# Kernel tuning notes

Measured on AMD Instinct MI355X. Metric: run time of the kernel, lower is better.

The kernel has to match this reference:

```python
import jax, jax.numpy as jnp
import numpy as np

B, S, E = 8, 4096, 128
H, O = 64, 64  # attention_hidden_dim, out_dim


def setup_inputs() -> dict:
    key = jax.random.key(0)
    ks = jax.random.split(key, 4)
    x = jax.random.normal(ks[0], (B, S, E), dtype=jnp.float32)
    Wq = jax.random.normal(ks[1], (E, H), dtype=jnp.float32) * (1.0 / np.sqrt(E))
    Wk = jax.random.normal(ks[2], (E, H), dtype=jnp.float32) * (1.0 / np.sqrt(E))
    Wv = jax.random.normal(ks[3], (E, O), dtype=jnp.float32) * (1.0 / np.sqrt(E))
    bq = jnp.zeros((H,), dtype=jnp.float32)
    bk = jnp.zeros((H,), dtype=jnp.float32)
    bv = jnp.zeros((O,), dtype=jnp.float32)
    return {"x": x, "Wq": Wq, "bq": bq, "Wk": Wk, "bk": bk, "Wv": Wv, "bv": bv}


def reference(x, Wq, bq, Wk, bk, Wv, bv):
    # Batched version of the per-sample loop: q = x@Wq+bq, etc.
    q = jnp.einsum("bse,eh->bsh", x, Wq) + bq   # [B,S,H]
    k = jnp.einsum("bse,eh->bsh", x, Wk) + bk   # [B,S,H]
    v = jnp.einsum("bse,eo->bso", x, Wv) + bv   # [B,S,O]
    scores = jnp.einsum("bqh,bkh->bqk", q, k)   # QK^T per sample, [B,S,S]
    attn = jax.nn.softmax(scores, axis=-1)       # softmax over key dim
    out = jnp.einsum("bqk,bko->bqo", attn, v)   # [B,S,O]
    return out
```

## Files before the change

### kernel.cpp

```cpp
#include <hip/hip_runtime.h>
#include <math.h>

#define BB 8
#define SS 4096
#define EE 128
#define HH 64
#define NT 16
#define LOG2E 1.44269504088896f

typedef _Float16 f16;
typedef __attribute__((ext_vector_type(8))) _Float16 f16x8;
typedef __attribute__((ext_vector_type(4))) float f32x4;

__device__ __forceinline__ unsigned int pk2h(float a, float b) {
    return __builtin_bit_cast(unsigned int, __builtin_amdgcn_cvt_pkrtz(a, b));
}

__device__ __forceinline__ void tile_barrier() {
    asm volatile("s_waitcnt lgkmcnt(0)" ::: "memory");
    __builtin_amdgcn_s_barrier();
    __builtin_amdgcn_sched_barrier(0);
}

__global__ __launch_bounds__(256) void wtrans_kernel(
    const float* __restrict__ Wq, const float* __restrict__ Wk,
    const float* __restrict__ Wv, f16* __restrict__ Wt)
{
    const int idx = blockIdx.x * 256 + threadIdx.x;
    if (idx >= 192 * 128) return;
    const int col = idx >> 7, e = idx & 127;
    const float v = (col < 64)  ? Wq[e * 64 + col] * LOG2E
                  : (col < 128) ? Wk[e * 64 + (col - 64)]
                                : Wv[e * 64 + (col - 128)];
    Wt[col * 128 + e] = (f16)v;
}

__global__ __launch_bounds__(256) void qkv_kernel(
    const float* __restrict__ x, const f16* __restrict__ Wt,
    const float* __restrict__ bq, const float* __restrict__ bk,
    const float* __restrict__ bv,
    f16* __restrict__ Q, f16* __restrict__ K, f16* __restrict__ Vt)
{
    __shared__ __align__(16) short xs[64 * EE];
    const int tid = threadIdx.x;
    const long rowbase = (long)blockIdx.x * 64;

    {
        const float4* xg = (const float4*)(x + rowbase * EE);
#pragma unroll
        for (int j = 0; j < 8; ++j) {
            const int eidx = tid * 32 + j * 4;
            const float4 v = xg[eidx >> 2];
            unsigned long long pk =
                (unsigned long long)pk2h(v.x, v.y) |
                ((unsigned long long)pk2h(v.z, v.w) << 32);
            const int row = eidx >> 7;
            const int off = (row * 256 + (eidx & 127) * 2) ^ ((row & 7) << 4);
            *(unsigned long long*)((char*)xs + off) = pk;
        }
    }
    __syncthreads();

    const int lane = tid & 63;
    const int wid  = tid >> 6;
    const int ln15 = lane & 15;
    const int lg   = lane >> 4;

    f16x8 xa[4];
    {
        const int row = wid * 16 + ln15;
        const int swz = (row & 7) << 4;
#pragma unroll
        for (int s = 0; s < 4; ++s)
            xa[s] = *(const f16x8*)((const char*)xs + ((row * 256 + lg * 16 + s * 64) ^ swz));
    }

    f32x4 acc[12];
#pragma unroll
    for (int ct = 0; ct < 12; ++ct) acc[ct] = (f32x4){0.f, 0.f, 0.f, 0.f};

#pragma unroll
    for (int ct = 0; ct < 12; ++ct) {
        const f16* wtp = Wt + (ct * 16 + ln15) * 128 + lg * 8;
#pragma unroll
        for (int s = 0; s < 4; ++s) {
            const f16x8 wb = *(const f16x8*)(wtp + s * 32);
            acc[ct] = __builtin_amdgcn_mfma_f32_16x16x32_f16(xa[s], wb, acc[ct], 0, 0, 0);
        }
    }

    const long grow0 = rowbase + wid * 16 + 4 * lg;
#pragma unroll
    for (int ct = 0; ct < 4; ++ct) {
        const int col = ct * 16 + ln15;
        const float b = bq[col] * LOG2E;
#pragma unroll
        for (int r = 0; r < 4; ++r)
            Q[(grow0 + r) * HH + col] = (f16)(acc[ct][r] + b);
    }
#pragma unroll
    for (int ct = 4; ct < 8; ++ct) {
        const int col = (ct - 4) * 16 + ln15;
        const float b = bk[col];
#pragma unroll
        for (int r = 0; r < 4; ++r)
            K[(grow0 + r) * HH + col] = (f16)(acc[ct][r] + b);
    }
    {
        const long batch = rowbase >> 12;
        const long inrow = (rowbase & 4095) + wid * 16 + 4 * lg;
#pragma unroll
        for (int ct = 8; ct < 12; ++ct) {
            const int o = (ct - 8) * 16 + ln15;
            const float b = bv[o];
            unsigned long long pk =
                (unsigned long long)pk2h(acc[ct][0] + b, acc[ct][1] + b) |
                ((unsigned long long)pk2h(acc[ct][2] + b, acc[ct][3] + b) << 32);
            *(unsigned long long*)(Vt + ((long)batch * HH + o) * SS + inrow) = pk;
        }
    }
}

__global__ __launch_bounds__(256, 4) void flash_kernel(
    const f16* __restrict__ Q, const f16* __restrict__ K,
    const f16* __restrict__ Vt, f16* __restrict__ Onorm,
    float* __restrict__ lse)
{
    __shared__ __align__(16) short k_s[2][64 * HH];
    __shared__ __align__(16) short v_s[2][64 * HH];
    __shared__ __align__(16) short p_s[4 * 16 * HH];

    const int tid  = threadIdx.x;
    const int lane = tid & 63;
    const int wid  = tid >> 6;
    const int ln15 = lane & 15;
    const int lg   = lane >> 4;
    const int batch = blockIdx.x & 7;
    const int rest  = blockIdx.x >> 3;
    const int split = rest & 3;
    const int qtile = rest >> 2;
    const int k0base = split * (SS / 4);

    f16x8 qf[2];
    {
        const long qrow = (long)batch * SS + qtile * 64 + wid * 16 + ln15;
        const f16* qp = Q + qrow * HH + lg * 8;
        qf[0] = *(const f16x8*)(qp);
        qf[1] = *(const f16x8*)(qp + 32);
    }

    f32x4 oacc[4];
#pragma unroll
    for (int ot = 0; ot < 4; ++ot) oacc[ot] = (f32x4){0.f, 0.f, 0.f, 0.f};
    float m = -1e30f, l = 0.f;

    short* pw = p_s + wid * (16 * HH);
    const int swq = (ln15 & 7) << 4;

    const int row0 = tid >> 3;
    const int row1 = row0 + 32;
    const int cc0  = (tid & 7) * 16;
    const int dk0 = (row0 * 128 + cc0) ^ ((row0 & 7) << 4);
    const int dk1 = (row1 * 128 + cc0) ^ ((row1 & 7) << 4);

    const uint4* kb  = (const uint4*)(K + ((long)batch * SS + k0base) * HH);
    const f16* vbase = Vt + (long)batch * HH * SS + k0base + (tid & 7) * 8;

    uint4 kA0, kA1, vA0, vA1, kB0, kB1, vB0, vB1;

#define LOADT(t, k0r, k1r, v0r, v1r)                                   \
    do {                                                               \
        const uint4* kp = kb + (t) * 512 + tid;                        \
        k0r = kp[0];                                                   \
        k1r = kp[256];                                                 \
        const f16* vp = vbase + (t) * 64 + (long)row0 * SS;            \
        v0r = *(const uint4*)vp;                                       \
        v1r = *(const uint4*)(vp + 32 * SS);                           \
    } while (0)

#define WRITET(buf, k0r, k1r, v0r, v1r)                                \
    do {                                                               \
        *(uint4*)((char*)k_s[buf] + dk0) = k0r;                        \
        *(uint4*)((char*)k_s[buf] + dk1) = k1r;                        \
        *(uint4*)((char*)v_s[buf] + dk0) = v0r;                        \
        *(uint4*)((char*)v_s[buf] + dk1) = v1r;                        \
    } while (0)

    auto compute = [&](int cur) __attribute__((always_inline)) {
        const short* ks = k_s[cur];
        const short* vs = v_s[cur];

        f32x4 sacc[4];
        __builtin_amdgcn_s_setprio(1);
#pragma unroll
        for (int kt = 0; kt < 4; ++kt) {
            f32x4 a = (f32x4){0.f, 0.f, 0.f, 0.f};
            const int key = kt * 16 + ln15;
            const int rb = key * 128, swz = (key & 7) << 4;
            const f16x8 ka0 = *(const f16x8*)((const char*)ks + ((rb + lg * 16) ^ swz));
            const f16x8 ka1 = *(const f16x8*)((const char*)ks + ((rb + lg * 16 + 64) ^ swz));
            a = __builtin_amdgcn_mfma_f32_16x16x32_f16(ka0, qf[0], a, 0, 0, 0);
            a = __builtin_amdgcn_mfma_f32_16x16x32_f16(ka1, qf[1], a, 0, 0, 0);
            sacc[kt] = a;
        }
        __builtin_amdgcn_s_setprio(0);

        float t0 = fmaxf(fmaxf(sacc[0][0], sacc[0][1]), sacc[0][2]);
        float t1 = fmaxf(fmaxf(sacc[0][3], sacc[1][0]), sacc[1][1]);
        float t2 = fmaxf(fmaxf(sacc[1][2], sacc[1][3]), sacc[2][0]);
        float t3 = fmaxf(fmaxf(sacc[2][1], sacc[2][2]), sacc[2][3]);
        float t4 = fmaxf(fmaxf(sacc[3][0], sacc[3][1]), sacc[3][2]);
        float tm = fmaxf(fmaxf(fmaxf(t0, t1), t2), fmaxf(fmaxf(t3, t4), sacc[3][3]));
        tm = fmaxf(tm, __shfl_xor(tm, 16));
        tm = fmaxf(tm, __shfl_xor(tm, 32));
        if (!__all(tm <= m + 11.5f)) {
            const float mn = fmaxf(m, tm);
            const float alpha = __builtin_amdgcn_exp2f(m - mn);
            l *= alpha;
#pragma unroll
            for (int r = 0; r < 4; ++r) {
                const float ar = __shfl(alpha, lg * 4 + r);
                oacc[0][r] *= ar; oacc[1][r] *= ar;
                oacc[2][r] *= ar; oacc[3][r] *= ar;
            }
            m = mn;
        }

        float ps = 0.f;
#pragma unroll
        for (int kt = 0; kt < 4; ++kt)
#pragma unroll
            for (int r = 0; r < 4; ++r) {
                const float pv = __builtin_amdgcn_exp2f(sacc[kt][r] - m);
                sacc[kt][r] = pv;
                ps += pv;
            }
        ps += __shfl_xor(ps, 16);
        ps += __shfl_xor(ps, 32);
        l += ps;

#pragma unroll
        for (int kt = 0; kt < 4; ++kt) {
            uint2 pk;
            pk.x = pk2h(sacc[kt][0], sacc[kt][1]);
            pk.y = pk2h(sacc[kt][2], sacc[kt][3]);
            const int key = kt * 16 + lg * 4;
            *(uint2*)((char*)pw + ((ln15 * 128 + key * 2) ^ swq)) = pk;
        }

        __builtin_amdgcn_s_setprio(1);
#pragma unroll
        for (int s = 0; s < 2; ++s) {
            const f16x8 pa = *(const f16x8*)((const char*)pw + ((ln15 * 128 + lg * 16 + s * 64) ^ swq));
#pragma unroll
            for (int ot = 0; ot < 4; ++ot) {
                const int o = ot * 16 + ln15;
                const f16x8 vb = *(const f16x8*)((const char*)vs + ((o * 128 + lg * 16 + s * 64) ^ ((o & 7) << 4)));
                oacc[ot] = __builtin_amdgcn_mfma_f32_16x16x32_f16(pa, vb, oacc[ot], 0, 0, 0);
            }
        }
        __builtin_amdgcn_s_setprio(0);
    };

    LOADT(0, kA0, kA1, vA0, vA1);
    WRITET(0, kA0, kA1, vA0, vA1);
    LOADT(1, kA0, kA1, vA0, vA1);
    __syncthreads();

    for (int t = 0; t < NT; t += 2) {
        compute(0);
        if (t + 2 < NT) LOADT(t + 2, kB0, kB1, vB0, vB1);
        WRITET(1, kA0, kA1, vA0, vA1);
        tile_barrier();

        compute(1);
        if (t + 3 < NT) LOADT(t + 3, kA0, kA1, vA0, vA1);
        if (t + 2 < NT) WRITET(0, kB0, kB1, vB0, vB1);
        tile_barrier();
    }
#undef LOADT
#undef WRITET

    const float linv = 1.0f / l;
    const long ridx = (long)split * (BB * SS) + (long)batch * SS + qtile * 64 + wid * 16;
#pragma unroll
    for (int r = 0; r < 4; ++r) {
        const float ir = __shfl(linv, lg * 4 + r);
        f16* op = Onorm + (ridx + lg * 4 + r) * HH + ln15;
        op[0]  = (f16)(oacc[0][r] * ir);
        op[16] = (f16)(oacc[1][r] * ir);
        op[32] = (f16)(oacc[2][r] * ir);
        op[48] = (f16)(oacc[3][r] * ir);
    }
    if (lg == 0)
        lse[ridx + ln15] = m + __builtin_amdgcn_logf(l);
}

__global__ __launch_bounds__(256) void merge_kernel(
    const f16* __restrict__ Onorm, const float* __restrict__ lse,
    float* __restrict__ Out)
{
    const int gid = blockIdx.x * 256 + threadIdx.x;
    const long row = gid >> 3;
    const int c0 = (gid & 7) * 8;
    const long NR = (long)BB * SS;

    float ls[4];
#pragma unroll
    for (int i = 0; i < 4; ++i) ls[i] = lse[i * NR + row];
    const float M = fmaxf(fmaxf(ls[0], ls[1]), fmaxf(ls[2], ls[3]));
    float g[4], denom = 0.f;
#pragma unroll
    for (int i = 0; i < 4; ++i) { g[i] = __builtin_amdgcn_exp2f(ls[i] - M); denom += g[i]; }
    const float inv = 1.0f / denom;

    float acc[8];
#pragma unroll
    for (int j = 0; j < 8; ++j) acc[j] = 0.f;
#pragma unroll
    for (int i = 0; i < 4; ++i) {
        const f16x8 o = *(const f16x8*)(Onorm + (i * NR + row) * HH + c0);
#pragma unroll
        for (int j = 0; j < 8; ++j) acc[j] = fmaf(g[i], (float)o[j], acc[j]);
    }
    float4 r0, r1;
    r0.x = acc[0] * inv; r0.y = acc[1] * inv; r0.z = acc[2] * inv; r0.w = acc[3] * inv;
    r1.x = acc[4] * inv; r1.y = acc[5] * inv; r1.z = acc[6] * inv; r1.w = acc[7] * inv;
    float4* dst = (float4*)(Out + row * HH + c0);
    dst[0] = r0;
    dst[1] = r1;
}

extern "C" void kernel_launch(void* const* d_in, const int* in_sizes, int n_in,
                              void* d_out, int out_size, void* d_ws, size_t ws_size,
                              hipStream_t stream) {
    const float* x  = (const float*)d_in[0];
    const float* Wq = (const float*)d_in[1];
    const float* bq = (const float*)d_in[2];
    const float* Wk = (const float*)d_in[3];
    const float* bk = (const float*)d_in[4];
    const float* Wv = (const float*)d_in[5];
    const float* bv = (const float*)d_in[6];
    float* out = (float*)d_out;

    const size_t NTOK = (size_t)BB * SS;
    f16* Q  = (f16*)d_ws;
    f16* K  = Q + NTOK * HH;
    f16* Vt = K + NTOK * HH;
    f16* Wt = Vt + NTOK * HH;
    f16* Onorm = Wt + 192 * 128;
    float* lse = (float*)(Onorm + 4 * NTOK * HH);

    wtrans_kernel<<<96, 256, 0, stream>>>(Wq, Wk, Wv, Wt);
    qkv_kernel<<<BB * SS / 64, 256, 0, stream>>>(x, Wt, bq, bk, bv, Q, K, Vt);
    flash_kernel<<<BB * 4 * (SS / 64), 256, 0, stream>>>(Q, K, Vt, Onorm, lse);
    merge_kernel<<<BB * SS * 8 / 256, 256, 0, stream>>>(Onorm, lse, out);
}
```

Baseline: 89.11 us.

## Stream K/V tiles directly into LDS with async global_load_lds copies

Replaces the register-staged K/V tile loads (global load to VGPRs, then ds_write into swizzled LDS) with direct global-to-LDS async copies issued per wave. The double-buffer schedule now issues the next tile's copy before computing the current tile and waits on vmcnt at each barrier. This removes the register staging and LDS write instructions and frees VGPRs. In exchange, prefetch distance drops to one tile and every barrier must wait on outstanding global loads, which may expose memory latency.

```diff
diff --git a/kernel.cpp b/kernel.cpp
--- a/kernel.cpp
+++ b/kernel.cpp
@@ -16,8 +16,14 @@
     return __builtin_bit_cast(unsigned int, __builtin_amdgcn_cvt_pkrtz(a, b));
 }
 
-__device__ __forceinline__ void tile_barrier() {
-    asm volatile("s_waitcnt lgkmcnt(0)" ::: "memory");
+__device__ __forceinline__ void async_copy16(void* lds, const void* g) {
+    __builtin_amdgcn_global_load_lds(
+        (const __attribute__((address_space(1))) void*)g,
+        (__attribute__((address_space(3))) void*)lds, 16, 0, 0);
+}
+
+__device__ __forceinline__ void vm_barrier() {
+    asm volatile("s_waitcnt vmcnt(0) lgkmcnt(0)" ::: "memory");
     __builtin_amdgcn_s_barrier();
     __builtin_amdgcn_sched_barrier(0);
 }
@@ -157,34 +163,24 @@
     short* pw = p_s + wid * (16 * HH);
     const int swq = (ln15 & 7) << 4;
 
-    const int row0 = tid >> 3;
-    const int row1 = row0 + 32;
-    const int cc0  = (tid & 7) * 16;
-    const int dk0 = (row0 * 128 + cc0) ^ ((row0 & 7) << 4);
-    const int dk1 = (row1 * 128 + cc0) ^ ((row1 & 7) << 4);
-
-    const uint4* kb  = (const uint4*)(K + ((long)batch * SS + k0base) * HH);
-    const f16* vbase = Vt + (long)batch * HH * SS + k0base + (tid & 7) * 8;
-
-    uint4 kA0, kA1, vA0, vA1, kB0, kB1, vB0, vB1;
-
-#define LOADT(t, k0r, k1r, v0r, v1r)                                   \
-    do {                                                               \
-        const uint4* kp = kb + (t) * 512 + tid;                        \
-        k0r = kp[0];                                                   \
-        k1r = kp[256];                                                 \
-        const f16* vp = vbase + (t) * 64 + (long)row0 * SS;            \
-        v0r = *(const uint4*)vp;                                       \
-        v1r = *(const uint4*)(vp + 32 * SS);                           \
-    } while (0)
-
-#define WRITET(buf, k0r, k1r, v0r, v1r)                                \
-    do {                                                               \
-        *(uint4*)((char*)k_s[buf] + dk0) = k0r;                        \
-        *(uint4*)((char*)k_s[buf] + dk1) = k1r;                        \
-        *(uint4*)((char*)v_s[buf] + dk0) = v0r;                        \
-        *(uint4*)((char*)v_s[buf] + dk1) = v1r;                        \
-    } while (0)
+    const int crow = lane >> 3;
+    const int ccs  = ((lane & 7) * 16) ^ (crow << 4);
+    const int row0 = wid * 16 + crow;
+    const char* kgb = (const char*)(K + ((long)batch * SS + k0base) * HH);
+    const char* vgb = (const char*)(Vt + (long)batch * HH * SS);
+    const long koff = (long)row0 * 128 + ccs;
+    const long voff = (long)row0 * (SS * 2) + k0base * 2 + ccs;
+
+    auto issue = [&](int t, int b) __attribute__((always_inline)) {
+        char* kl = (char*)k_s[b] + wid * 2048;
+        char* vl = (char*)v_s[b] + wid * 2048;
+        const char* kg = kgb + (long)t * (64 * 128) + koff;
+        const char* vg = vgb + (long)t * 128 + voff;
+        async_copy16(kl,        kg);
+        async_copy16(kl + 1024, kg + 1024);
+        async_copy16(vl,        vg);
+        async_copy16(vl + 1024, vg + 8 * (SS * 2));
+    };
 
     auto compute = [&](int cur) __attribute__((always_inline)) {
         const short* ks = k_s[cur];
@@ -262,24 +258,17 @@
         __builtin_amdgcn_s_setprio(0);
     };
 
-    LOADT(0, kA0, kA1, vA0, vA1);
-    WRITET(0, kA0, kA1, vA0, vA1);
-    LOADT(1, kA0, kA1, vA0, vA1);
-    __syncthreads();
+    issue(0, 0);
+    vm_barrier();
 
     for (int t = 0; t < NT; t += 2) {
+        issue(t + 1, 1);
         compute(0);
-        if (t + 2 < NT) LOADT(t + 2, kB0, kB1, vB0, vB1);
-        WRITET(1, kA0, kA1, vA0, vA1);
-        tile_barrier();
-
+        vm_barrier();
+        if (t + 2 < NT) issue(t + 2, 0);
         compute(1);
-        if (t + 3 < NT) LOADT(t + 3, kA0, kA1, vA0, vA1);
-        if (t + 2 < NT) WRITET(0, kB0, kB1, vB0, vB1);
-        tile_barrier();
-    }
-#undef LOADT
-#undef WRITET
+        vm_barrier();
+    }
 
     const float linv = 1.0f / l;
     const long ridx = (long)split * (BB * SS) + (long)batch * SS + qtile * 64 + wid * 16;
```

New measurement: 90.93 us. 2.0% more time.
